# Kernel optimization log

Measured on AMD Instinct MI355X. Metric: run time of the kernel, lower is better.

## Reference

```python
import jax, jax.numpy as jnp
import numpy as np

B, T, C = 32, 512, 32
D, H, DFF, NL = 512, 8, 2048, 3
P, STRIDE, PAD = 16, 8, 8
N = (T - P) // STRIDE + 2  # 64 patches
E = D // H


def _sinusoidal_pe(n, d):
    pos = np.arange(n, dtype=np.float32)[:, None]
    div = np.exp(np.arange(0, d, 2, dtype=np.float32) * -(np.log(10000.0) / d))
    pe = np.zeros((n, d), np.float32)
    pe[:, 0::2] = np.sin(pos * div)
    pe[:, 1::2] = np.cos(pos * div)
    return jnp.asarray(pe)


def setup_inputs() -> dict:
    key = jax.random.key(0)
    ks = jax.random.split(key, 16)
    s = 0.02
    inp = {
        'x_enc': jax.random.normal(ks[0], (B, T, C), jnp.float32),
        'W_val': jax.random.normal(ks[1], (P, D), jnp.float32) * s,
        'Wq': jax.random.normal(ks[2], (NL, D, D), jnp.float32) * s,
        'bq': jnp.zeros((NL, D), jnp.float32),
        'Wk': jax.random.normal(ks[3], (NL, D, D), jnp.float32) * s,
        'bk': jnp.zeros((NL, D), jnp.float32),
        'Wv': jax.random.normal(ks[4], (NL, D, D), jnp.float32) * s,
        'bv': jnp.zeros((NL, D), jnp.float32),
        'Wo': jax.random.normal(ks[5], (NL, D, D), jnp.float32) * s,
        'bo': jnp.zeros((NL, D), jnp.float32),
        'Wc1': jax.random.normal(ks[6], (NL, D, DFF), jnp.float32) * s,
        'bc1': jnp.zeros((NL, DFF), jnp.float32),
        'Wc2': jax.random.normal(ks[7], (NL, DFF, D), jnp.float32) * s,
        'bc2': jnp.zeros((NL, D), jnp.float32),
        'ln1_g': jnp.ones((NL, D), jnp.float32),
        'ln1_b': jnp.zeros((NL, D), jnp.float32),
        'ln2_g': jnp.ones((NL, D), jnp.float32),
        'ln2_b': jnp.zeros((NL, D), jnp.float32),
        'bn_g': jnp.ones((D,), jnp.float32),
        'bn_b': jnp.zeros((D,), jnp.float32),
        'W_head': jax.random.normal(ks[8], (D * N, T), jnp.float32) * s,
        'b_head': jnp.zeros((T,), jnp.float32),
    }
    return inp


def _ln(x, g, b, eps=1e-5):
    m = x.mean(-1, keepdims=True)
    v = ((x - m) ** 2).mean(-1, keepdims=True)
    return (x - m) / jnp.sqrt(v + eps) * g + b


def reference(x_enc, W_val, Wq, bq, Wk, bk, Wv, bv, Wo, bo, Wc1, bc1, Wc2, bc2,
              ln1_g, ln1_b, ln2_g, ln2_b, bn_g, bn_b, W_head, b_head):
    pe = _sinusoidal_pe(N, D)
    # instance normalization over time (means detached, as in torch .detach())
    means = jax.lax.stop_gradient(x_enc.mean(axis=1, keepdims=True))
    x = x_enc - means
    stdev = jnp.sqrt(x.var(axis=1, keepdims=True) + 1e-5)  # [B,1,C]
    x = x / stdev
    x = x.transpose(0, 2, 1)  # [B, C, T]
    # replication pad right by PAD, then unfold into patches [B,C,N,P]
    x = jnp.concatenate([x, jnp.broadcast_to(x[..., -1:], x.shape[:-1] + (PAD,))], axis=-1)
    idx = jnp.arange(N)[:, None] * STRIDE + jnp.arange(P)[None, :]
    xp = x[..., idx]
    tok = xp.reshape(B * C, N, P) @ W_val + pe  # [B*C, N, D]

    scale = 1.0 / np.sqrt(E).astype(np.float32)
    for i in range(NL):
        q = (tok @ Wq[i] + bq[i]).reshape(-1, N, H, E)
        k = (tok @ Wk[i] + bk[i]).reshape(-1, N, H, E)
        v = (tok @ Wv[i] + bv[i]).reshape(-1, N, H, E)
        scores = jnp.einsum('blhe,bshe->bhls', q, k)
        A = jax.nn.softmax(scale * scores, axis=-1)
        V = jnp.einsum('bhls,bshd->blhd', A, v).reshape(-1, N, D)
        tok = tok + (V @ Wo[i] + bo[i])
        y = _ln(tok, ln1_g[i], ln1_b[i])
        y = jax.nn.gelu(y @ Wc1[i] + bc1[i], approximate=False) @ Wc2[i] + bc2[i]
        tok = _ln(tok + y, ln2_g[i], ln2_b[i])

    # BatchNorm1d over d_model channels (batch statistics, biased variance)
    m = tok.mean(axis=(0, 1))
    var = tok.var(axis=(0, 1))
    tok = (tok - m) / jnp.sqrt(var + 1e-5) * bn_g + bn_b

    enc = tok.reshape(B, C, N, D).transpose(0, 1, 3, 2).reshape(B, C, D * N)
    dec = enc @ W_head + b_head          # [B, C, T]
    dec = dec.transpose(0, 2, 1)          # [B, T, C]
    dec = dec * stdev[:, 0, :][:, None, :] + means[:, 0, :][:, None, :]
    return dec
```

## Files before the change

kernel.cpp:

```cpp
#include <hip/hip_runtime.h>
#include <math.h>

namespace {
constexpr int kB = 32, kT = 512, kC = 32, kD = 512, kDFF = 2048, kNL = 3;
constexpr int kP = 16, kStride = 8, kN = 64;
constexpr int kR = kB * kC;
constexpr int kM = kR * kN;
constexpr size_t kWbElems = (size_t)1536 * 512 + 512 * 512 + 2048 * 512 + 512 * 2048;
}

typedef unsigned short u16;
typedef __attribute__((ext_vector_type(8))) short short8;
typedef __attribute__((ext_vector_type(4))) float f32x4;

__device__ __forceinline__ float b2f(u16 u) {
    return __uint_as_float(((unsigned int)u) << 16);
}
__device__ __forceinline__ u16 f2b(float f) {
    unsigned int x = __float_as_uint(f);
    return (u16)((x + 0x7fffu + ((x >> 16) & 1u)) >> 16);
}

__device__ __forceinline__ void async_copy16(const void* g, void* l) {
    __builtin_amdgcn_global_load_lds(
        (const __attribute__((address_space(1))) unsigned int*)g,
        (__attribute__((address_space(3))) unsigned int*)l, 16, 0, 0);
}

__global__ void fill_kernel(float* __restrict__ p, float val, int n)
{
    int i = blockIdx.x * blockDim.x + threadIdx.x;
    if (i < n) p[i] = val;
}

__global__ __launch_bounds__(256) void instnorm_stats_kernel(
    const float* __restrict__ x, float* __restrict__ means, float* __restrict__ stdev)
{
    int b = blockIdx.x;
    int c = threadIdx.x & 31;
    int g = threadIdx.x >> 5;
    float s = 0.f, sq = 0.f;
    for (int t = g; t < kT; t += 8) {
        float v = x[(size_t)(b * kT + t) * kC + c];
        s += v; sq += v * v;
    }
    __shared__ float ss[8][32], ssq[8][32];
    ss[g][c] = s; ssq[g][c] = sq;
    __syncthreads();
    if (g == 0) {
        float S = 0.f, SQ = 0.f;
        for (int i = 0; i < 8; i++) { S += ss[i][c]; SQ += ssq[i][c]; }
        float m = S / kT;
        float var = SQ / kT - m * m;
        means[b * kC + c] = m;
        stdev[b * kC + c] = sqrtf(var + 1e-5f);
    }
}

__global__ __launch_bounds__(256) void patch_embed_kernel(
    const float* __restrict__ x, const float* __restrict__ Wval,
    const float* __restrict__ means, const float* __restrict__ stdev,
    u16* __restrict__ tok)
{
    int m = blockIdx.x;
    int r = m >> 6, n = m & 63;
    int b = r >> 5, c = r & 31;
    __shared__ float patch[kP];
    if (threadIdx.x < kP) {
        int t = n * kStride + threadIdx.x;
        if (t > kT - 1) t = kT - 1;
        patch[threadIdx.x] = (x[(size_t)(b * kT + t) * kC + c] - means[r]) / stdev[r];
    }
    __syncthreads();
    for (int d = threadIdx.x; d < kD; d += 256) {
        float acc = 0.f;
        #pragma unroll
        for (int p = 0; p < kP; p++) acc += patch[p] * Wval[p * kD + d];
        int j = d >> 1;
        float freq = expf(-(float)(2 * j) * (9.210340371976184f / (float)kD));
        float ang = (float)n * freq;
        float pe = (d & 1) ? cosf(ang) : sinf(ang);
        tok[(size_t)m * kD + d] = f2b(acc + pe);
    }
}

__global__ __launch_bounds__(256) void transpose_cvt_kernel(
    const float* __restrict__ in, u16* __restrict__ outp,
    int ldi, int ldo, int zin, int zout)
{
    __shared__ float tile[64][65];
    const float* ib = in + (size_t)blockIdx.z * zin;
    u16* ob = outp + (size_t)blockIdx.z * zout;
    int k0 = blockIdx.x * 64, n0 = blockIdx.y * 64;
    int tn = threadIdx.x & 63, tk0 = threadIdx.x >> 6;
    #pragma unroll
    for (int kk = tk0; kk < 64; kk += 4)
        tile[kk][tn] = ib[(size_t)(k0 + kk) * ldi + n0 + tn];
    __syncthreads();
    int wk = threadIdx.x & 63, wn0 = threadIdx.x >> 6;
    #pragma unroll
    for (int nn = wn0; nn < 64; nn += 4)
        ob[(size_t)(n0 + nn) * ldo + k0 + wk] = f2b(tile[wk][nn]);
}

template<int EPI>
__global__ __launch_bounds__(256) void mfma_gemm(
    const u16* __restrict__ A, const u16* __restrict__ B,
    const float* __restrict__ bias, const float* __restrict__ auxb1,
    const float* __restrict__ auxb2,
    u16* __restrict__ C0, u16* __restrict__ C1, u16* __restrict__ C2,
    float* __restrict__ fout, const float* __restrict__ stdev,
    int K, int lda, int ldb, int ldc)
{
    __shared__ u16 As[128 * 32];
    __shared__ u16 Bs[128 * 32];
    const int tid = threadIdx.x;
    const int lane = tid & 63;
    const int wave = tid >> 6;
    const int row0 = blockIdx.y * 128;
    const int col0 = blockIdx.x * 128;
    const size_t zoff = (size_t)blockIdx.z * K;

    const int stRow = (wave << 4) + (lane >> 2);
    const int stCol = ((lane & 3) ^ ((lane >> 2) & 3)) << 3;
    const u16* Ag = A + (size_t)(row0 + stRow) * lda + zoff + stCol;
    const u16* Bg = B + (size_t)(col0 + stRow) * ldb + zoff + stCol;
    u16* AsW = As + (wave << 4) * 32;
    u16* BsW = Bs + (wave << 4) * 32;

    const int fm = lane & 15;
    const int fkx = ((lane >> 4) ^ (lane & 3)) << 3;
    const int wm = wave & 1, wn = wave >> 1;

    f32x4 acc[4][4];
    #pragma unroll
    for (int i = 0; i < 4; i++)
        #pragma unroll
        for (int j = 0; j < 4; j++)
            acc[i][j] = (f32x4){0.f, 0.f, 0.f, 0.f};

    for (int kb = 0; kb < K; kb += 32) {
        __syncthreads();
        async_copy16(Ag + kb, AsW);
        async_copy16(Ag + kb + (size_t)64 * lda, AsW + 64 * 32);
        async_copy16(Bg + kb, BsW);
        async_copy16(Bg + kb + (size_t)64 * ldb, BsW + 64 * 32);
        __syncthreads();
        short8 af[4], bfr[4];
        #pragma unroll
        for (int mi = 0; mi < 4; mi++)
            af[mi] = *(const short8*)&As[((wm << 6) + (mi << 4) + fm) * 32 + fkx];
        #pragma unroll
        for (int ni = 0; ni < 4; ni++)
            bfr[ni] = *(const short8*)&Bs[((wn << 6) + (ni << 4) + fm) * 32 + fkx];
        #pragma unroll
        for (int mi = 0; mi < 4; mi++)
            #pragma unroll
            for (int ni = 0; ni < 4; ni++)
                acc[mi][ni] = __builtin_amdgcn_mfma_f32_16x16x32_bf16(
                    af[mi], bfr[ni], acc[mi][ni], 0, 0, 0);
    }

    const int er = (lane >> 4) << 2;
    const int ec = lane & 15;
    u16* dsel = C0;
    const float* bsel = bias;
    if (EPI == 0) {
        int sub = col0 >> 9;
        dsel = (sub == 0) ? C0 : ((sub == 1) ? C1 : C2);
        bsel = (sub == 0) ? bias : ((sub == 1) ? auxb1 : auxb2);
    }
    #pragma unroll
    for (int mi = 0; mi < 4; mi++) {
        #pragma unroll
        for (int ni = 0; ni < 4; ni++) {
            #pragma unroll
            for (int i = 0; i < 4; i++) {
                int r = row0 + (wm << 6) + (mi << 4) + er + i;
                int cc = col0 + (wn << 6) + (ni << 4) + ec;
                float v = acc[mi][ni][i];
                if (EPI == 0) {
                    int cl = cc & 511;
                    dsel[(size_t)r * 512 + cl] = f2b(v + bsel[cl]);
                } else if (EPI == 1) {
                    size_t o = (size_t)r * ldc + cc;
                    float bb = bias ? bias[cc] : 0.f;
                    C0[o] = f2b(b2f(C0[o]) + v + bb);
                } else if (EPI == 2) {
                    size_t o = (size_t)r * ldc + cc;
                    float z = v + bias[cc];
                    C0[o] = f2b(0.5f * z * (1.f + erff(z * 0.7071067811865475f)));
                } else {
                    float vv = v * stdev[r];
                    atomicAdd(&fout[(((size_t)(r >> 5) * kT + cc) << 5) + (r & 31)], vv);
                }
            }
        }
    }
}

__global__ __launch_bounds__(256) void attn_mfma_kernel(
    u16* __restrict__ qbuf, const u16* __restrict__ kbuf,
    const u16* __restrict__ vbuf)
{
    __shared__ u16 P[4][64 * 64];
    const int tid = threadIdx.x;
    const int wave = tid >> 6, lane = tid & 63;
    const int quad = lane >> 4, l15 = lane & 15;
    const size_t base = (size_t)blockIdx.x * 64 * kD;
    u16* Pw = P[wave];

    for (int hh = 0; hh < 2; hh++) {
        const int h = wave * 2 + hh;
        const u16* qh = qbuf + base + h * 64;
        const u16* kh = kbuf + base + h * 64;
        const u16* vh = vbuf + base + h * 64;

        short8 af[4][2], bf[4][2];
        #pragma unroll
        for (int mi = 0; mi < 4; mi++)
            #pragma unroll
            for (int kt = 0; kt < 2; kt++)
                af[mi][kt] = *(const short8*)(qh + (size_t)(mi * 16 + l15) * kD
                                              + kt * 32 + quad * 8);
        #pragma unroll
        for (int ni = 0; ni < 4; ni++)
            #pragma unroll
            for (int kt = 0; kt < 2; kt++)
                bf[ni][kt] = *(const short8*)(kh + (size_t)(ni * 16 + l15) * kD
                                              + kt * 32 + quad * 8);
        f32x4 S[4][4];
        #pragma unroll
        for (int mi = 0; mi < 4; mi++)
            #pragma unroll
            for (int ni = 0; ni < 4; ni++)
                S[mi][ni] = (f32x4){0.f, 0.f, 0.f, 0.f};
        #pragma unroll
        for (int mi = 0; mi < 4; mi++)
            #pragma unroll
            for (int ni = 0; ni < 4; ni++) {
                S[mi][ni] = __builtin_amdgcn_mfma_f32_16x16x32_bf16(
                    af[mi][0], bf[ni][0], S[mi][ni], 0, 0, 0);
                S[mi][ni] = __builtin_amdgcn_mfma_f32_16x16x32_bf16(
                    af[mi][1], bf[ni][1], S[mi][ni], 0, 0, 0);
            }

        #pragma unroll
        for (int mi = 0; mi < 4; mi++) {
            #pragma unroll
            for (int i = 0; i < 4; i++) {
                float mx = -1e30f;
                #pragma unroll
                for (int ni = 0; ni < 4; ni++) {
                    float v = S[mi][ni][i] * 0.125f;
                    S[mi][ni][i] = v;
                    mx = fmaxf(mx, v);
                }
                #pragma unroll
                for (int off = 1; off < 16; off <<= 1)
                    mx = fmaxf(mx, __shfl_xor(mx, off));
                float sum = 0.f;
                #pragma unroll
                for (int ni = 0; ni < 4; ni++) {
                    float e = expf(S[mi][ni][i] - mx);
                    S[mi][ni][i] = e;
                    sum += e;
                }
                #pragma unroll
                for (int off = 1; off < 16; off <<= 1)
                    sum += __shfl_xor(sum, off);
                float inv = 1.f / sum;
                #pragma unroll
                for (int ni = 0; ni < 4; ni++)
                    Pw[(mi * 16 + quad * 4 + i) * 64 + ni * 16 + l15] =
                        f2b(S[mi][ni][i] * inv);
            }
        }
        __syncthreads();

        short8 bv[4][2];
        #pragma unroll
        for (int ni = 0; ni < 4; ni++)
            #pragma unroll
            for (int kt = 0; kt < 2; kt++)
                #pragma unroll
                for (int j = 0; j < 8; j++)
                    bv[ni][kt][j] = (short)vh[(size_t)(kt * 32 + quad * 8 + j) * kD
                                              + ni * 16 + l15];
        short8 pa[4][2];
        #pragma unroll
        for (int mi = 0; mi < 4; mi++)
            #pragma unroll
            for (int kt = 0; kt < 2; kt++)
                pa[mi][kt] = *(const short8*)&Pw[(mi * 16 + l15) * 64
                                                 + kt * 32 + quad * 8];
        f32x4 O[4][4];
        #pragma unroll
        for (int mi = 0; mi < 4; mi++)
            #pragma unroll
            for (int ni = 0; ni < 4; ni++)
                O[mi][ni] = (f32x4){0.f, 0.f, 0.f, 0.f};
        #pragma unroll
        for (int mi = 0; mi < 4; mi++)
            #pragma unroll
            for (int ni = 0; ni < 4; ni++) {
                O[mi][ni] = __builtin_amdgcn_mfma_f32_16x16x32_bf16(
                    pa[mi][0], bv[ni][0], O[mi][ni], 0, 0, 0);
                O[mi][ni] = __builtin_amdgcn_mfma_f32_16x16x32_bf16(
                    pa[mi][1], bv[ni][1], O[mi][ni], 0, 0, 0);
            }
        u16* qo = qbuf + base + h * 64;
        #pragma unroll
        for (int mi = 0; mi < 4; mi++)
            #pragma unroll
            for (int ni = 0; ni < 4; ni++)
                #pragma unroll
                for (int i = 0; i < 4; i++)
                    qo[(size_t)(mi * 16 + quad * 4 + i) * kD + ni * 16 + l15] =
                        f2b(O[mi][ni][i]);
        __syncthreads();
    }
}

__global__ __launch_bounds__(256) void ln_kernel(
    const u16* __restrict__ x, const float* __restrict__ g,
    const float* __restrict__ bb, u16* __restrict__ y)
{
    size_t row = (size_t)blockIdx.x * 4 + (threadIdx.x >> 6);
    int lane = threadIdx.x & 63;
    float v[8];
    float s = 0.f;
    #pragma unroll
    for (int i = 0; i < 8; i++) {
        v[i] = b2f(x[row * kD + lane + i * 64]);
        s += v[i];
    }
    #pragma unroll
    for (int off = 32; off; off >>= 1) s += __shfl_xor(s, off);
    float mean = s * (1.f / kD);
    float sq = 0.f;
    #pragma unroll
    for (int i = 0; i < 8; i++) { float d = v[i] - mean; sq += d * d; }
    #pragma unroll
    for (int off = 32; off; off >>= 1) sq += __shfl_xor(sq, off);
    float inv = 1.f / sqrtf(sq * (1.f / kD) + 1e-5f);
    #pragma unroll
    for (int i = 0; i < 8; i++) {
        int d = lane + i * 64;
        y[row * kD + d] = f2b((v[i] - mean) * inv * g[d] + bb[d]);
    }
}

__global__ void zero_kernel(float* __restrict__ p, int n)
{
    int i = blockIdx.x * blockDim.x + threadIdx.x;
    if (i < n) p[i] = 0.f;
}

__global__ __launch_bounds__(512) void bn_stats_kernel(
    const u16* __restrict__ tok, float* __restrict__ sums, float* __restrict__ sumsq)
{
    int d = threadIdx.x;
    float s = 0.f, sq = 0.f;
    int row0 = blockIdx.x * 256;
    for (int row = row0; row < row0 + 256; row++) {
        float v = b2f(tok[(size_t)row * kD + d]);
        s += v; sq += v * v;
    }
    atomicAdd(&sums[d], s);
    atomicAdd(&sumsq[d], sq);
}

__global__ __launch_bounds__(512) void bn_final_kernel(
    const float* __restrict__ sums, const float* __restrict__ sumsq,
    const float* __restrict__ g, const float* __restrict__ bb,
    float* __restrict__ scale, float* __restrict__ shift)
{
    int d = threadIdx.x;
    float mean = sums[d] / (float)kM;
    float var = sumsq[d] / (float)kM - mean * mean;
    float sc = g[d] / sqrtf(var + 1e-5f);
    scale[d] = sc;
    shift[d] = bb[d] - mean * sc;
}

__global__ __launch_bounds__(256) void bn_apply_kernel(
    u16* __restrict__ tok, const float* __restrict__ scale,
    const float* __restrict__ shift)
{
    size_t i = (size_t)blockIdx.x * 256 + threadIdx.x;
    int d = (int)(i & 511);
    tok[i] = f2b(b2f(tok[i]) * scale[d] + shift[d]);
}

__global__ __launch_bounds__(256) void head_init_kernel(
    float* __restrict__ out, const float* __restrict__ b_head,
    const float* __restrict__ stdev, const float* __restrict__ means)
{
    int i = blockIdx.x * 256 + threadIdx.x;
    int c = i & 31, t = (i >> 5) & 511, b = i >> 14;
    int r = b * 32 + c;
    out[i] = b_head[t] * stdev[r] + means[r];
}

extern "C" void kernel_launch(void* const* d_in, const int* in_sizes, int n_in,
                              void* d_out, int out_size, void* d_ws, size_t ws_size,
                              hipStream_t stream)
{
    const float* x_enc  = (const float*)d_in[0];
    const float* W_val  = (const float*)d_in[1];
    const float* Wq     = (const float*)d_in[2];
    const float* bq     = (const float*)d_in[3];
    const float* Wk     = (const float*)d_in[4];
    const float* bk     = (const float*)d_in[5];
    const float* Wv     = (const float*)d_in[6];
    const float* bv     = (const float*)d_in[7];
    const float* Wo     = (const float*)d_in[8];
    const float* bo     = (const float*)d_in[9];
    const float* Wc1    = (const float*)d_in[10];
    const float* bc1    = (const float*)d_in[11];
    const float* Wc2    = (const float*)d_in[12];
    const float* bc2    = (const float*)d_in[13];
    const float* ln1_g  = (const float*)d_in[14];
    const float* ln1_b  = (const float*)d_in[15];
    const float* ln2_g  = (const float*)d_in[16];
    const float* ln2_b  = (const float*)d_in[17];
    const float* bn_g   = (const float*)d_in[18];
    const float* bn_b   = (const float*)d_in[19];
    const float* W_head = (const float*)d_in[20];
    const float* b_head = (const float*)d_in[21];
    float* out = (float*)d_out;

    const size_t tailBytes = (2 * kR + 4 * kD) * sizeof(float);
    const size_t headWb = (size_t)512 * 32768;
    int CH = 0; size_t unit = 0, region = 0;
    const int cands[4] = {1024, 512, 256, 128};
    for (int ci = 0; ci < 4; ci++) {
        size_t u = (size_t)cands[ci] * 64 * kD;
        size_t reg = 3 * u + kWbElems;
        if (reg < headWb) reg = headWb;
        size_t need = ((size_t)kM * kD + reg) * 2 + tailBytes;
        if (need <= ws_size) { CH = cands[ci]; unit = u; region = reg; break; }
    }
    if (CH == 0) {
        hipLaunchKernelGGL(fill_kernel, dim3((out_size + 255) / 256), dim3(256), 0,
                           stream, out, 1.0e6f, out_size);
        return;
    }
    const int nch = kR / CH;
    const int chRows = CH * 64;

    u16* tokb = (u16*)d_ws;
    u16* s0  = tokb + (size_t)kM * kD;
    u16* s1  = s0 + unit;
    u16* s2  = s1 + unit;
    u16* wbL = s2 + unit;
    u16* wbH = s0;
    u16* wQKV = wbL;
    u16* wO   = wQKV + (size_t)1536 * 512;
    u16* wC1  = wO + (size_t)512 * 512;
    u16* wC2  = wC1 + (size_t)2048 * 512;
    float* tail = (float*)(s0 + region);
    float* means    = tail;
    float* stdevp   = means + kR;
    float* bn_sums  = stdevp + kR;
    float* bn_sumsq = bn_sums + kD;
    float* bn_scale = bn_sumsq + kD;
    float* bn_shift = bn_scale + kD;

    hipLaunchKernelGGL(instnorm_stats_kernel, dim3(kB), dim3(256), 0, stream,
                       x_enc, means, stdevp);
    hipLaunchKernelGGL(patch_embed_kernel, dim3(kM), dim3(256), 0, stream,
                       x_enc, W_val, means, stdevp, tokb);

    const dim3 blk(256);
    const dim3 tr8(8, 8, 1);
    const int mt = chRows / 128;

    for (int i = 0; i < kNL; i++) {
        const float* Wq_i = Wq + (size_t)i * kD * kD;
        const float* Wk_i = Wk + (size_t)i * kD * kD;
        const float* Wv_i = Wv + (size_t)i * kD * kD;
        const float* Wo_i = Wo + (size_t)i * kD * kD;
        const float* Wc1_i = Wc1 + (size_t)i * kD * kDFF;
        const float* Wc2_i = Wc2 + (size_t)i * kDFF * kD;
        const float* bq_i = bq + i * kD, *bk_i = bk + i * kD, *bv_i = bv + i * kD;

        hipLaunchKernelGGL(transpose_cvt_kernel, tr8, blk, 0, stream,
                           Wq_i, wQKV, kD, kD, 0, 0);
        hipLaunchKernelGGL(transpose_cvt_kernel, tr8, blk, 0, stream,
                           Wk_i, wQKV + (size_t)512 * 512, kD, kD, 0, 0);
        hipLaunchKernelGGL(transpose_cvt_kernel, tr8, blk, 0, stream,
                           Wv_i, wQKV + (size_t)1024 * 512, kD, kD, 0, 0);
        hipLaunchKernelGGL(transpose_cvt_kernel, tr8, blk, 0, stream,
                           Wo_i, wO, kD, kD, 0, 0);
        hipLaunchKernelGGL(transpose_cvt_kernel, dim3(8, 32, 1), blk, 0, stream,
                           Wc1_i, wC1, kDFF, kD, 0, 0);
        hipLaunchKernelGGL(transpose_cvt_kernel, dim3(32, 8, 1), blk, 0, stream,
                           Wc2_i, wC2, kD, kDFF, 0, 0);

        for (int ch = 0; ch < nch; ch++) {
            u16* tokc = tokb + (size_t)ch * chRows * kD;
            hipLaunchKernelGGL(mfma_gemm<0>, dim3(12, mt, 1), blk, 0, stream,
                               tokc, wQKV, bq_i, bk_i, bv_i, s0, s1, s2,
                               nullptr, nullptr, kD, kD, kD, kD);
            hipLaunchKernelGGL(attn_mfma_kernel, dim3(CH), blk, 0, stream,
                               s0, s1, s2);
            hipLaunchKernelGGL(mfma_gemm<1>, dim3(4, mt, 1), blk, 0, stream,
                               s0, wO, bo + i * kD, nullptr, nullptr,
                               tokc, nullptr, nullptr, nullptr, nullptr,
                               kD, kD, kD, kD);
            hipLaunchKernelGGL(ln_kernel, dim3(chRows / 4), blk, 0, stream,
                               tokc, ln1_g + i * kD, ln1_b + i * kD, s0);
            for (int half = 0; half < 2; half++) {
                const u16* wc1h = wC1 + (size_t)half * 1024 * 512;
                const u16* wc2h = wC2 + (size_t)half * 1024;
                const float* bc1h = bc1 + (size_t)i * kDFF + half * 1024;
                hipLaunchKernelGGL(mfma_gemm<2>, dim3(8, mt, 1), blk, 0, stream,
                                   s0, wc1h, bc1h, nullptr, nullptr,
                                   s1, nullptr, nullptr, nullptr, nullptr,
                                   kD, kD, kD, 1024);
                hipLaunchKernelGGL(mfma_gemm<1>, dim3(4, mt, 1), blk, 0, stream,
                                   s1, wc2h, (half == 0) ? (bc2 + i * kD) : nullptr,
                                   nullptr, nullptr, tokc, nullptr, nullptr,
                                   nullptr, nullptr, 1024, 1024, kDFF, kD);
            }
            hipLaunchKernelGGL(ln_kernel, dim3(chRows / 4), blk, 0, stream,
                               tokc, ln2_g + i * kD, ln2_b + i * kD, tokc);
        }
    }

    hipLaunchKernelGGL(zero_kernel, dim3(1), dim3(1024), 0, stream, bn_sums, 2 * kD);
    hipLaunchKernelGGL(bn_stats_kernel, dim3(kM / 256), dim3(512), 0, stream,
                       tokb, bn_sums, bn_sumsq);
    hipLaunchKernelGGL(bn_final_kernel, dim3(1), dim3(512), 0, stream,
                       bn_sums, bn_sumsq, bn_g, bn_b, bn_scale, bn_shift);
    hipLaunchKernelGGL(bn_apply_kernel, dim3((int)((size_t)kM * kD / 256)), blk, 0,
                       stream, tokb, bn_scale, bn_shift);

    hipLaunchKernelGGL(transpose_cvt_kernel, dim3(8, 8, 64), blk, 0, stream,
                       W_head, wbH, 64 * 512, 32768, 512, 512);
    hipLaunchKernelGGL(head_init_kernel, dim3(out_size / 256), blk, 0, stream,
                       out, b_head, stdevp, means);
    hipLaunchKernelGGL(mfma_gemm<3>, dim3(4, 8, 8), blk, 0, stream,
                       tokb, wbH, nullptr, nullptr, nullptr,
                       nullptr, nullptr, nullptr, out, stdevp,
                       4096, 32768, 32768, kT);
}
```

Before: 3.856 ms.

## Replace GEMM with 256x256-tile double-buffered 8-wave pipelined MFMA kernel

Replaces the 128x128, 4-wave, single-buffered GEMM with a 256x256-tile, 8-wave kernel. It uses 128 KB of double-buffered LDS, interleaves async global->LDS loads with MFMA quadrants, and raises MFMA priority with setprio. It also adds an XCD-aware workgroup remapping to improve L2 locality, and re-splits the head GEMM's K into 32 chunks. The aim is to overlap memory with compute and raise arithmetic intensity. The cost is higher register pressure (8x4 accumulators), fewer workgroups per chunk, and a requirement that K be a multiple of 128.

```diff
diff --git a/kernel.cpp b/kernel.cpp
--- a/kernel.cpp
+++ b/kernel.cpp
@@ -104,7 +104,7 @@
 }
 
 template<int EPI>
-__global__ __launch_bounds__(256) void mfma_gemm(
+__global__ __launch_bounds__(512, 2) void gemm8(
     const u16* __restrict__ A, const u16* __restrict__ B,
     const float* __restrict__ bias, const float* __restrict__ auxb1,
     const float* __restrict__ auxb2,
@@ -112,53 +112,125 @@
     float* __restrict__ fout, const float* __restrict__ stdev,
     int K, int lda, int ldb, int ldc)
 {
-    __shared__ u16 As[128 * 32];
-    __shared__ u16 Bs[128 * 32];
-    const int tid = threadIdx.x;
+    __shared__ u16 sm[65536];
+    u16* const bufA0 = sm;
+    u16* const bufB0 = sm + 16384;
+    u16* const bufA1 = sm + 32768;
+    u16* const bufB1 = sm + 49152;
+
+    const int tid  = threadIdx.x;
     const int lane = tid & 63;
     const int wave = tid >> 6;
-    const int row0 = blockIdx.y * 128;
-    const int col0 = blockIdx.x * 128;
+    const int wm   = wave >> 2;
+    const int wn   = wave & 3;
+
+    const int nwg  = gridDim.x * gridDim.y;
+    const int orig = blockIdx.y * gridDim.x + blockIdx.x;
+    const int qq = nwg >> 3, rr = nwg & 7;
+    const int xcd = orig & 7, loc = orig >> 3;
+    const int wg  = (xcd < rr) ? (xcd * (qq + 1) + loc)
+                               : (rr * (qq + 1) + (xcd - rr) * qq + loc);
+    const int row0 = (wg / gridDim.x) * 256;
+    const int col0 = (wg % gridDim.x) * 256;
     const size_t zoff = (size_t)blockIdx.z * K;
 
-    const int stRow = (wave << 4) + (lane >> 2);
-    const int stCol = ((lane & 3) ^ ((lane >> 2) & 3)) << 3;
-    const u16* Ag = A + (size_t)(row0 + stRow) * lda + zoff + stCol;
-    const u16* Bg = B + (size_t)(col0 + stRow) * ldb + zoff + stCol;
-    u16* AsW = As + (wave << 4) * 32;
-    u16* BsW = Bs + (wave << 4) * 32;
-
-    const int fm = lane & 15;
-    const int fkx = ((lane >> 4) ^ (lane & 3)) << 3;
-    const int wm = wave & 1, wn = wave >> 1;
-
-    f32x4 acc[4][4];
-    #pragma unroll
-    for (int i = 0; i < 4; i++)
+    const int srow = (wave << 3) + (lane >> 3);
+    const int scol = ((lane & 7) ^ (lane >> 3)) << 3;
+    const u16* const Ag = A + (size_t)(row0 + srow) * lda + zoff + scol;
+    const u16* const Bg = B + (size_t)(col0 + srow) * ldb + zoff + scol;
+    const int lw = wave << 3;
+
+#define STAGE_A(BUF, R0, T) do { \
+        const u16* g_ = Ag + (size_t)(R0) * lda + (T) * 64; \
+        u16* l_ = bufA##BUF + (((R0) + lw) << 6); \
+        async_copy16(g_, l_); \
+        async_copy16(g_ + (size_t)64 * lda, l_ + (64 << 6)); \
+    } while (0)
+#define STAGE_B(BUF, R0, T) do { \
+        const u16* g_ = Bg + (size_t)(R0) * ldb + (T) * 64; \
+        u16* l_ = bufB##BUF + (((R0) + lw) << 6); \
+        async_copy16(g_, l_); \
+        async_copy16(g_ + (size_t)64 * ldb, l_ + (64 << 6)); \
+    } while (0)
+
+    const int fr = lane & 15;
+    const int pc = (lane >> 4) ^ (lane & 7);
+    const int a0 = ((wm << 7) + fr) * 64 + pc * 8;
+    const int a1 = ((wm << 7) + fr) * 64 + (pc ^ 4) * 8;
+    const int b0 = ((wn << 6) + fr) * 64 + pc * 8;
+    const int b1 = ((wn << 6) + fr) * 64 + (pc ^ 4) * 8;
+
+    short8 af[8][2], bfr[4][2];
+    f32x4 acc[8][4];
+    #pragma unroll
+    for (int i = 0; i < 8; i++)
         #pragma unroll
         for (int j = 0; j < 4; j++)
             acc[i][j] = (f32x4){0.f, 0.f, 0.f, 0.f};
 
-    for (int kb = 0; kb < K; kb += 32) {
-        __syncthreads();
-        async_copy16(Ag + kb, AsW);
-        async_copy16(Ag + kb + (size_t)64 * lda, AsW + 64 * 32);
-        async_copy16(Bg + kb, BsW);
-        async_copy16(Bg + kb + (size_t)64 * ldb, BsW + 64 * 32);
-        __syncthreads();
-        short8 af[4], bfr[4];
-        #pragma unroll
-        for (int mi = 0; mi < 4; mi++)
-            af[mi] = *(const short8*)&As[((wm << 6) + (mi << 4) + fm) * 32 + fkx];
-        #pragma unroll
-        for (int ni = 0; ni < 4; ni++)
-            bfr[ni] = *(const short8*)&Bs[((wn << 6) + (ni << 4) + fm) * 32 + fkx];
-        #pragma unroll
-        for (int mi = 0; mi < 4; mi++)
-            #pragma unroll
-            for (int ni = 0; ni < 4; ni++)
-                acc[mi][ni] = __builtin_amdgcn_mfma_f32_16x16x32_bf16(
-                    af[mi], bfr[ni], acc[mi][ni], 0, 0, 0);
+#define RD_A(BUF, MH) do { \
+        _Pragma("unroll") \
+        for (int mi_ = 0; mi_ < 4; mi_++) { \
+            af[(MH)*4 + mi_][0] = *(const short8*)&bufA##BUF[a0 + (((MH)*4 + mi_) << 10)]; \
+            af[(MH)*4 + mi_][1] = *(const short8*)&bufA##BUF[a1 + (((MH)*4 + mi_) << 10)]; \
+        } \
+    } while (0)
+#define RD_B(BUF, NH) do { \
+        _Pragma("unroll") \
+        for (int ni_ = 0; ni_ < 2; ni_++) { \
+            bfr[(NH)*2 + ni_][0] = *(const short8*)&bufB##BUF[b0 + (((NH)*2 + ni_) << 10)]; \
+            bfr[(NH)*2 + ni_][1] = *(const short8*)&bufB##BUF[b1 + (((NH)*2 + ni_) << 10)]; \
+        } \
+    } while (0)
+#define MFMA_Q(MH, NH) do { \
+        __builtin_amdgcn_s_setprio(1); \
+        _Pragma("unroll") \
+        for (int mi_ = 0; mi_ < 4; mi_++) \
+            _Pragma("unroll") \
+            for (int ni_ = 0; ni_ < 2; ni_++) { \
+                acc[(MH)*4 + mi_][(NH)*2 + ni_] = __builtin_amdgcn_mfma_f32_16x16x32_bf16( \
+                    af[(MH)*4 + mi_][0], bfr[(NH)*2 + ni_][0], \
+                    acc[(MH)*4 + mi_][(NH)*2 + ni_], 0, 0, 0); \
+                acc[(MH)*4 + mi_][(NH)*2 + ni_] = __builtin_amdgcn_mfma_f32_16x16x32_bf16( \
+                    af[(MH)*4 + mi_][1], bfr[(NH)*2 + ni_][1], \
+                    acc[(MH)*4 + mi_][(NH)*2 + ni_], 0, 0, 0); \
+            } \
+        __builtin_amdgcn_s_setprio(0); \
+    } while (0)
+#define BAR() __builtin_amdgcn_s_barrier()
+#define VM_FENCE(N) asm volatile("s_waitcnt vmcnt(" #N ")" ::: "memory")
+
+    STAGE_A(0, 0, 0);  STAGE_A(0, 128, 0);
+    STAGE_B(0, 0, 0);  STAGE_B(0, 128, 0);
+    STAGE_A(1, 0, 1);  STAGE_A(1, 128, 1);
+    VM_FENCE(4);
+    BAR();
+
+    const int nIter = K >> 7;
+    for (int it = 0; it < nIter; it++) {
+        const int t1 = 2 * it + 1, t2 = 2 * it + 2, t3 = 2 * it + 3;
+        const bool full = (it < nIter - 1);
+        RD_A(0, 0); RD_B(0, 0);
+        STAGE_B(1, 0, t1);
+        BAR(); MFMA_Q(0, 0); BAR();
+        RD_A(0, 1); RD_B(0, 1);
+        STAGE_B(1, 128, t1);
+        BAR(); MFMA_Q(1, 0); BAR();
+        if (full) STAGE_A(0, 0, t2);
+        BAR(); MFMA_Q(0, 1); BAR();
+        if (full) { STAGE_A(0, 128, t2); VM_FENCE(4); }
+        else      { VM_FENCE(0); }
+        BAR(); MFMA_Q(1, 1); BAR();
+        RD_A(1, 0); RD_B(1, 0);
+        if (full) STAGE_B(0, 0, t2);
+        BAR(); MFMA_Q(0, 0); BAR();
+        RD_A(1, 1); RD_B(1, 1);
+        if (full) STAGE_B(0, 128, t2);
+        BAR(); MFMA_Q(1, 0); BAR();
+        if (full) STAGE_A(1, 0, t3);
+        BAR(); MFMA_Q(0, 1); BAR();
+        if (full) { STAGE_A(1, 128, t3); VM_FENCE(4); }
+        BAR(); MFMA_Q(1, 1); BAR();
     }
 
     const int er = (lane >> 4) << 2;
@@ -171,12 +243,12 @@
         bsel = (sub == 0) ? bias : ((sub == 1) ? auxb1 : auxb2);
     }
     #pragma unroll
-    for (int mi = 0; mi < 4; mi++) {
+    for (int mi = 0; mi < 8; mi++) {
         #pragma unroll
         for (int ni = 0; ni < 4; ni++) {
             #pragma unroll
             for (int i = 0; i < 4; i++) {
-                int r = row0 + (wm << 6) + (mi << 4) + er + i;
+                int r  = row0 + (wm << 7) + (mi << 4) + er + i;
                 int cc = col0 + (wn << 6) + (ni << 4) + ec;
                 float v = acc[mi][ni][i];
                 if (EPI == 0) {
@@ -184,8 +256,8 @@
                     dsel[(size_t)r * 512 + cl] = f2b(v + bsel[cl]);
                 } else if (EPI == 1) {
                     size_t o = (size_t)r * ldc + cc;
-                    float bb = bias ? bias[cc] : 0.f;
-                    C0[o] = f2b(b2f(C0[o]) + v + bb);
+                    float bb2 = bias ? bias[cc] : 0.f;
+                    C0[o] = f2b(b2f(C0[o]) + v + bb2);
                 } else if (EPI == 2) {
                     size_t o = (size_t)r * ldc + cc;
                     float z = v + bias[cc];
@@ -197,6 +269,13 @@
             }
         }
     }
+#undef STAGE_A
+#undef STAGE_B
+#undef RD_A
+#undef RD_B
+#undef MFMA_Q
+#undef BAR
+#undef VM_FENCE
 }
 
 __global__ __launch_bounds__(256) void attn_mfma_kernel(
@@ -474,8 +553,9 @@
                        x_enc, W_val, means, stdevp, tokb);
 
     const dim3 blk(256);
+    const dim3 blk512(512);
     const dim3 tr8(8, 8, 1);
-    const int mt = chRows / 128;
+    const int mt256 = chRows / 256;
 
     for (int i = 0; i < kNL; i++) {
         const float* Wq_i = Wq + (size_t)i * kD * kD;
@@ -501,12 +581,12 @@
 
         for (int ch = 0; ch < nch; ch++) {
             u16* tokc = tokb + (size_t)ch * chRows * kD;
-            hipLaunchKernelGGL(mfma_gemm<0>, dim3(12, mt, 1), blk, 0, stream,
+            hipLaunchKernelGGL((gemm8<0>), dim3(6, mt256, 1), blk512, 0, stream,
                                tokc, wQKV, bq_i, bk_i, bv_i, s0, s1, s2,
                                nullptr, nullptr, kD, kD, kD, kD);
             hipLaunchKernelGGL(attn_mfma_kernel, dim3(CH), blk, 0, stream,
                                s0, s1, s2);
-            hipLaunchKernelGGL(mfma_gemm<1>, dim3(4, mt, 1), blk, 0, stream,
+            hipLaunchKernelGGL((gemm8<1>), dim3(2, mt256, 1), blk512, 0, stream,
                                s0, wO, bo + i * kD, nullptr, nullptr,
                                tokc, nullptr, nullptr, nullptr, nullptr,
                                kD, kD, kD, kD);
@@ -516,11 +596,11 @@
                 const u16* wc1h = wC1 + (size_t)half * 1024 * 512;
                 const u16* wc2h = wC2 + (size_t)half * 1024;
                 const float* bc1h = bc1 + (size_t)i * kDFF + half * 1024;
-                hipLaunchKernelGGL(mfma_gemm<2>, dim3(8, mt, 1), blk, 0, stream,
+                hipLaunchKernelGGL((gemm8<2>), dim3(4, mt256, 1), blk512, 0, stream,
                                    s0, wc1h, bc1h, nullptr, nullptr,
                                    s1, nullptr, nullptr, nullptr, nullptr,
                                    kD, kD, kD, 1024);
-                hipLaunchKernelGGL(mfma_gemm<1>, dim3(4, mt, 1), blk, 0, stream,
+                hipLaunchKernelGGL((gemm8<1>), dim3(2, mt256, 1), blk512, 0, stream,
                                    s1, wc2h, (half == 0) ? (bc2 + i * kD) : nullptr,
                                    nullptr, nullptr, tokc, nullptr, nullptr,
                                    nullptr, nullptr, 1024, 1024, kDFF, kD);
@@ -542,8 +622,8 @@
                        W_head, wbH, 64 * 512, 32768, 512, 512);
     hipLaunchKernelGGL(head_init_kernel, dim3(out_size / 256), blk, 0, stream,
                        out, b_head, stdevp, means);
-    hipLaunchKernelGGL(mfma_gemm<3>, dim3(4, 8, 8), blk, 0, stream,
+    hipLaunchKernelGGL((gemm8<3>), dim3(2, 4, 32), blk512, 0, stream,
                        tokb, wbH, nullptr, nullptr, nullptr,
                        nullptr, nullptr, nullptr, out, stdevp,
-                       4096, 32768, 32768, kT);
-}
+                       1024, 32768, 32768, kT);
+}
```

Measured after the change: 3.743 ms. 1.03x faster.

## Double GEMM K-tile to 64 with new LDS swizzle and XCD-aware block remap

Applied to the files above, without the earlier changes.

The MFMA GEMM now stages a 64-wide K slice per iteration instead of 32. Each sync pair therefore covers two MFMA sub-steps, halving the number of barriers and load rounds. The LDS layout uses a new 8-way XOR swizzle to avoid bank conflicts. Workgroup IDs are remapped so consecutive tiles land on the same XCD for better L2 locality, at the cost of doubled shared memory per block, which may reduce occupancy.

```diff
diff --git a/kernel.cpp b/kernel.cpp
--- a/kernel.cpp
+++ b/kernel.cpp
@@ -21,7 +21,7 @@
     return (u16)((x + 0x7fffu + ((x >> 16) & 1u)) >> 16);
 }
 
-__device__ __forceinline__ void async_copy16(const void* g, void* l) {
+__device__ __forceinline__ void async_copy16(const u16* g, u16* l) {
     __builtin_amdgcn_global_load_lds(
         (const __attribute__((address_space(1))) unsigned int*)g,
         (__attribute__((address_space(3))) unsigned int*)l, 16, 0, 0);
@@ -112,26 +112,40 @@
     float* __restrict__ fout, const float* __restrict__ stdev,
     int K, int lda, int ldb, int ldc)
 {
-    __shared__ u16 As[128 * 32];
-    __shared__ u16 Bs[128 * 32];
-    const int tid = threadIdx.x;
+    __shared__ alignas(16) u16 As[128 * 64];
+    __shared__ alignas(16) u16 Bs[128 * 64];
+
+    const int tid  = threadIdx.x;
     const int lane = tid & 63;
     const int wave = tid >> 6;
-    const int row0 = blockIdx.y * 128;
-    const int col0 = blockIdx.x * 128;
+    const int wm   = wave >> 1;
+    const int wn   = wave & 1;
+
+    const int nwg  = gridDim.x * gridDim.y;
+    const int orig = blockIdx.y * gridDim.x + blockIdx.x;
+    const int qq = nwg >> 3, rr = nwg & 7;
+    const int xcd = orig & 7, loc = orig >> 3;
+    const int wg  = (xcd < rr) ? (xcd * (qq + 1) + loc)
+                               : (rr * (qq + 1) + (xcd - rr) * qq + loc);
+    const int row0 = (wg / gridDim.x) * 128;
+    const int col0 = (wg % gridDim.x) * 128;
     const size_t zoff = (size_t)blockIdx.z * K;
 
-    const int stRow = (wave << 4) + (lane >> 2);
-    const int stCol = ((lane & 3) ^ ((lane >> 2) & 3)) << 3;
-    const u16* Ag = A + (size_t)(row0 + stRow) * lda + zoff + stCol;
-    const u16* Bg = B + (size_t)(col0 + stRow) * ldb + zoff + stCol;
-    u16* AsW = As + (wave << 4) * 32;
-    u16* BsW = Bs + (wave << 4) * 32;
-
-    const int fm = lane & 15;
-    const int fkx = ((lane >> 4) ^ (lane & 3)) << 3;
-    const int wm = wave & 1, wn = wave >> 1;
-
+    const int srow = tid >> 3;
+    const int scol = (((tid & 7) ^ (srow & 7)) << 3);
+    const u16* const Ag = A + (size_t)(row0 + srow) * lda + zoff + scol;
+    const u16* const Bg = B + (size_t)(col0 + srow) * ldb + zoff + scol;
+    u16* const AsW = As + (wave << 9);
+    u16* const BsW = Bs + (wave << 9);
+
+    const int fr = lane & 15;
+    const int pc = (lane >> 4) ^ (lane & 7);
+    const int a0 = ((wm << 6) + fr) * 64 + (pc << 3);
+    const int a1 = ((wm << 6) + fr) * 64 + ((pc ^ 4) << 3);
+    const int b0 = ((wn << 6) + fr) * 64 + (pc << 3);
+    const int b1 = ((wn << 6) + fr) * 64 + ((pc ^ 4) << 3);
+
+    short8 af[4], bfr[4];
     f32x4 acc[4][4];
     #pragma unroll
     for (int i = 0; i < 4; i++)
@@ -139,20 +153,28 @@
         for (int j = 0; j < 4; j++)
             acc[i][j] = (f32x4){0.f, 0.f, 0.f, 0.f};
 
-    for (int kb = 0; kb < K; kb += 32) {
+    for (int kb = 0; kb < K; kb += 64) {
         __syncthreads();
-        async_copy16(Ag + kb, AsW);
-        async_copy16(Ag + kb + (size_t)64 * lda, AsW + 64 * 32);
-        async_copy16(Bg + kb, BsW);
-        async_copy16(Bg + kb + (size_t)64 * ldb, BsW + 64 * 32);
+        #pragma unroll
+        for (int c = 0; c < 4; c++) {
+            async_copy16(Ag + kb + (size_t)(c * 32) * lda, AsW + c * 2048);
+            async_copy16(Bg + kb + (size_t)(c * 32) * ldb, BsW + c * 2048);
+        }
         __syncthreads();
-        short8 af[4], bfr[4];
-        #pragma unroll
-        for (int mi = 0; mi < 4; mi++)
-            af[mi] = *(const short8*)&As[((wm << 6) + (mi << 4) + fm) * 32 + fkx];
-        #pragma unroll
-        for (int ni = 0; ni < 4; ni++)
-            bfr[ni] = *(const short8*)&Bs[((wn << 6) + (ni << 4) + fm) * 32 + fkx];
+        #pragma unroll
+        for (int mi = 0; mi < 4; mi++) af[mi]  = *(const short8*)&As[a0 + (mi << 10)];
+        #pragma unroll
+        for (int ni = 0; ni < 4; ni++) bfr[ni] = *(const short8*)&Bs[b0 + (ni << 10)];
+        #pragma unroll
+        for (int mi = 0; mi < 4; mi++)
+            #pragma unroll
+            for (int ni = 0; ni < 4; ni++)
+                acc[mi][ni] = __builtin_amdgcn_mfma_f32_16x16x32_bf16(
+                    af[mi], bfr[ni], acc[mi][ni], 0, 0, 0);
+        #pragma unroll
+        for (int mi = 0; mi < 4; mi++) af[mi]  = *(const short8*)&As[a1 + (mi << 10)];
+        #pragma unroll
+        for (int ni = 0; ni < 4; ni++) bfr[ni] = *(const short8*)&Bs[b1 + (ni << 10)];
         #pragma unroll
         for (int mi = 0; mi < 4; mi++)
             #pragma unroll
@@ -176,7 +198,7 @@
         for (int ni = 0; ni < 4; ni++) {
             #pragma unroll
             for (int i = 0; i < 4; i++) {
-                int r = row0 + (wm << 6) + (mi << 4) + er + i;
+                int r  = row0 + (wm << 6) + (mi << 4) + er + i;
                 int cc = col0 + (wn << 6) + (ni << 4) + ec;
                 float v = acc[mi][ni][i];
                 if (EPI == 0) {
@@ -184,8 +206,8 @@
                     dsel[(size_t)r * 512 + cl] = f2b(v + bsel[cl]);
                 } else if (EPI == 1) {
                     size_t o = (size_t)r * ldc + cc;
-                    float bb = bias ? bias[cc] : 0.f;
-                    C0[o] = f2b(b2f(C0[o]) + v + bb);
+                    float bb2 = bias ? bias[cc] : 0.f;
+                    C0[o] = f2b(b2f(C0[o]) + v + bb2);
                 } else if (EPI == 2) {
                     size_t o = (size_t)r * ldc + cc;
                     float z = v + bias[cc];
@@ -501,12 +523,12 @@
 
         for (int ch = 0; ch < nch; ch++) {
             u16* tokc = tokb + (size_t)ch * chRows * kD;
-            hipLaunchKernelGGL(mfma_gemm<0>, dim3(12, mt, 1), blk, 0, stream,
+            hipLaunchKernelGGL((mfma_gemm<0>), dim3(12, mt, 1), blk, 0, stream,
                                tokc, wQKV, bq_i, bk_i, bv_i, s0, s1, s2,
                                nullptr, nullptr, kD, kD, kD, kD);
             hipLaunchKernelGGL(attn_mfma_kernel, dim3(CH), blk, 0, stream,
                                s0, s1, s2);
-            hipLaunchKernelGGL(mfma_gemm<1>, dim3(4, mt, 1), blk, 0, stream,
+            hipLaunchKernelGGL((mfma_gemm<1>), dim3(4, mt, 1), blk, 0, stream,
                                s0, wO, bo + i * kD, nullptr, nullptr,
                                tokc, nullptr, nullptr, nullptr, nullptr,
                                kD, kD, kD, kD);
@@ -516,11 +538,11 @@
                 const u16* wc1h = wC1 + (size_t)half * 1024 * 512;
                 const u16* wc2h = wC2 + (size_t)half * 1024;
                 const float* bc1h = bc1 + (size_t)i * kDFF + half * 1024;
-                hipLaunchKernelGGL(mfma_gemm<2>, dim3(8, mt, 1), blk, 0, stream,
+                hipLaunchKernelGGL((mfma_gemm<2>), dim3(8, mt, 1), blk, 0, stream,
                                    s0, wc1h, bc1h, nullptr, nullptr,
                                    s1, nullptr, nullptr, nullptr, nullptr,
                                    kD, kD, kD, 1024);
-                hipLaunchKernelGGL(mfma_gemm<1>, dim3(4, mt, 1), blk, 0, stream,
+                hipLaunchKernelGGL((mfma_gemm<1>), dim3(4, mt, 1), blk, 0, stream,
                                    s1, wc2h, (half == 0) ? (bc2 + i * kD) : nullptr,
                                    nullptr, nullptr, tokc, nullptr, nullptr,
                                    nullptr, nullptr, 1024, 1024, kDFF, kD);
@@ -542,7 +564,7 @@
                        W_head, wbH, 64 * 512, 32768, 512, 512);
     hipLaunchKernelGGL(head_init_kernel, dim3(out_size / 256), blk, 0, stream,
                        out, b_head, stdevp, means);
-    hipLaunchKernelGGL(mfma_gemm<3>, dim3(4, 8, 8), blk, 0, stream,
+    hipLaunchKernelGGL((mfma_gemm<3>), dim3(4, 8, 8), blk, 0, stream,
                        tokb, wbH, nullptr, nullptr, nullptr,
                        nullptr, nullptr, nullptr, out, stdevp,
                        4096, 32768, 32768, kT);
```

Result: faster. 3.480 ms (-9.7%).
